# Performance work log

Hardware: AMD Instinct MI355X
Metric: run time of the kernel (lower is better)

Reference implementation:

```python
import jax, jax.numpy as jnp
import numpy as np
from math import sqrt

# ---- config (mirrors init_kwargs / input_specs) ----
B, N = 2, 2048
DIM, HEADS = 1024, 16
DH = DIM // HEADS
NUM_STEPS = 8
BETA = 1.0
SCALE = sqrt(DIM / 2 - 1)        # scale_from_dim(dim)
SCALE_HEAD = sqrt(DH / 2 - 1)    # scale_from_dim(dim_head)


def _normalize(x, eps=1e-12):
    # torch F.normalize(dim=-1): x / max(||x||, eps)
    n = jnp.linalg.norm(x, axis=-1, keepdims=True)
    return x / jnp.maximum(n, eps)


def _theta(x, J, m):
    # effective field: external field + attention-weighted coupling of magnetizations
    return x + jnp.einsum('bhij,bhjd->bhid', J, m)


def _magnetizations(theta, beta=BETA, scale=SCALE):
    # naive-MF single-site average for a vector spin on a sphere of radius `scale`
    # (steepest-descent closed form): m = beta*theta / (2 t),
    # t = (1 + sqrt(1 + beta^2 |theta|^2 / scale^2)) / 2
    # -> linear response beta*theta/2 for small fields, saturates at |m| = scale.
    h2 = jnp.sum(jnp.square(beta * theta), axis=-1, keepdims=True)
    t = 0.5 * (1.0 + jnp.sqrt(1.0 + h2 / (scale * scale)))
    return beta * theta / (2.0 * t)


def setup_inputs() -> dict:
    key = jax.random.key(0)
    k0, k1, k2, k3 = jax.random.split(key, 4)
    x = jax.random.normal(k0, (B, N, DIM), jnp.float32)
    w_qk = jax.random.normal(k1, (2 * DIM, DIM), jnp.float32) / sqrt(DIM)
    w1 = jax.random.normal(k2, (4 * DIM, DIM), jnp.float32) / sqrt(DIM)
    w2 = jax.random.normal(k3, (DIM, 4 * DIM), jnp.float32) / sqrt(4 * DIM)
    return {"x": x, "w_qk": w_qk, "w1": w1, "w2": w2}


def reference(x, w_qk, w1, w2):
    # pre_mix = Identity
    x = SCALE * _normalize(x)                         # [b,n,dim]
    qk = x @ w_qk.T                                   # [b,n,2*dim]
    q, k = jnp.split(qk, 2, axis=-1)
    ff = jax.nn.gelu(x @ w1.T, approximate=False) @ w2.T

    split = lambda t: t.reshape(B, N, HEADS, DH).transpose(0, 2, 1, 3)  # b h n d
    xh, q, k, ffh = map(split, (x, q, k, ff))
    q, k = _normalize(q), _normalize(k)
    sim = SCALE_HEAD * jnp.einsum('bhid,bhjd->bhij', q, k)
    attn = jax.nn.softmax(sim, axis=-1)               # [b,h,n,n] coupling matrix

    xf = xh + ffh                                     # external field
    # prev_mf_state.theta starts as ones(x.shape) on first call
    m0 = _magnetizations(jnp.ones_like(xf))

    # fixed-step mean-field iteration: m <- magnetizations(theta(x, attn, m))
    def body(m, _):
        m_next = _magnetizations(_theta(xf, attn, m))
        return m_next, None
    m, _ = jax.lax.scan(body, m0, None, length=NUM_STEPS)

    m = m.transpose(0, 2, 1, 3).reshape(B, N, DIM)    # merge heads
    # post_mix = Identity
    return m
```

## Files before the change

### kernel.cpp

```cpp
#include <hip/hip_runtime.h>
#include <hip/hip_bf16.h>
#include <math.h>

#define BQ 2
#define SEQ 2048
#define NDIM 1024
#define HEADS 16
#define DH 64
#define NSTEPS 8
#define SCALE 22.60530911f
#define SCALE_HEAD 5.567764363f
#define INV_SCALE2 (1.0f/511.0f)
#define EXS 8.0325527f

typedef unsigned short u16;
typedef unsigned char u8;
typedef long long i64;
typedef __attribute__((ext_vector_type(8))) short bf16x8;
typedef __attribute__((ext_vector_type(4))) float floatx4;
typedef __attribute__((ext_vector_type(2))) long long i64x2;

__device__ __forceinline__ float bf2f(u16 u) {
  union { unsigned int i; float f; } v; v.i = ((unsigned int)u) << 16; return v.f;
}
__device__ __forceinline__ u16 f2bf(float f) {
  union { float f; unsigned int i; } v; v.f = f;
  unsigned int x = v.i;
  return (u16)((x + 0x7fffu + ((x >> 16) & 1u)) >> 16);
}
#if __has_builtin(__builtin_amdgcn_exp2f)
__device__ __forceinline__ float exp2_raw(float x) { return __builtin_amdgcn_exp2f(x); }
#else
__device__ __forceinline__ float exp2_raw(float x) { return exp2f(x); }
#endif
#if __has_builtin(__builtin_amdgcn_rcpf)
__device__ __forceinline__ float rcp_raw(float x) { return __builtin_amdgcn_rcpf(x); }
#else
__device__ __forceinline__ float rcp_raw(float x) { return 1.0f/x; }
#endif

__device__ __forceinline__ float gelu_tanh(float v) {
  float v2 = v*v;
  float u = v * __builtin_fmaf(0.0356774081f, v2, 0.7978845608f);
  float t = exp2_raw(2.8853900817779268f * u);
  float th = (t - 1.0f) * rcp_raw(t + 1.0f);
  return 0.5f * v * (1.0f + th);
}

__device__ __forceinline__ int pk4_fp8(float a, float b, float c, float d) {
  int p = 0;
  p = __builtin_amdgcn_cvt_pk_fp8_f32(a, b, p, false);
  p = __builtin_amdgcn_cvt_pk_fp8_f32(c, d, p, true);
  return p;
}

#define GLD16(gp, lp) __builtin_amdgcn_global_load_lds( \
    (__attribute__((address_space(1))) void*)(gp),      \
    (__attribute__((address_space(3))) void*)(lp), 16, 0, 0)


__global__ void k_flag0(int* flag) { if (threadIdx.x == 0 && blockIdx.x == 0) *flag = 0; }

__global__ __launch_bounds__(256) void k_probe(const u16* __restrict__ x, int* __restrict__ flag) {
  int i = blockIdx.x * 256 + threadIdx.x;
  float v = bf2f(x[i]);
  if (!(fabsf(v) <= 1e4f)) atomicOr(flag, 1);
}

__global__ __launch_bounds__(256) void k_convert(const void* __restrict__ in, u16* __restrict__ outb,
                                                 const int* __restrict__ flag, int n) {
  int i = blockIdx.x * 256 + threadIdx.x;
  if (i >= n) return;
  if (*flag) outb[i] = f2bf(((const float*)in)[i]);
  else       outb[i] = ((const u16*)in)[i];
}

__global__ __launch_bounds__(256) void k_norm_scale(const u16* __restrict__ x, u16* __restrict__ xs) {
  __shared__ float red[256];
  int row = blockIdx.x;
  const u16* xr = x + (size_t)row * NDIM;
  u16* orow = xs + (size_t)row * NDIM;
  int t = threadIdx.x;
  float vals[4]; float s = 0.f;
#pragma unroll
  for (int e = 0; e < 4; e++) { float v = bf2f(xr[t + 256*e]); vals[e] = v; s += v*v; }
  red[t] = s; __syncthreads();
  for (int o = 128; o > 0; o >>= 1) { if (t < o) red[t] += red[t+o]; __syncthreads(); }
  float sc = SCALE / fmaxf(sqrtf(red[0]), 1e-12f);
#pragma unroll
  for (int e = 0; e < 4; e++) orow[t + 256*e] = f2bf(vals[e] * sc);
}

template<int OUT_BF16, int GELU, int ADDSRC>
__global__ __launch_bounds__(256) void k_gemm(const u16* __restrict__ A, const u16* __restrict__ W,
                                              float* __restrict__ Cf, u16* __restrict__ Cb,
                                              const u16* __restrict__ addsrc, int M, int N, int K) {
  __shared__ __align__(16) u16 As[128*32];
  __shared__ __align__(16) u16 Bs[128*32];
  int t = threadIdx.x;
  int w = t >> 6, L = t & 63;
  int quad = L >> 4, l15 = L & 15;
  int wr = w >> 1, wc = w & 1;
  int bm = blockIdx.x * 128, bn = blockIdx.y * 128;
  int srow = L >> 2, scol = (L & 3) * 8;
  floatx4 acc[4][4];
#pragma unroll
  for (int i = 0; i < 4; i++)
#pragma unroll
    for (int j = 0; j < 4; j++) acc[i][j] = (floatx4){0.f,0.f,0.f,0.f};

  for (int k0 = 0; k0 < K; k0 += 32) {
#pragma unroll
    for (int c = 0; c < 2; c++) {
      int r = c*64 + w*16 + srow;
      GLD16(A + (size_t)(bm + r)*K + k0 + scol, &As[(c*64 + w*16)*32]);
      GLD16(W + (size_t)(bn + r)*K + k0 + scol, &Bs[(c*64 + w*16)*32]);
    }
    __syncthreads();
    bf16x8 af[4], bfr[4];
#pragma unroll
    for (int mt = 0; mt < 4; mt++) af[mt]  = *(const bf16x8*)&As[(wr*64 + mt*16 + l15)*32 + quad*8];
#pragma unroll
    for (int nt = 0; nt < 4; nt++) bfr[nt] = *(const bf16x8*)&Bs[(wc*64 + nt*16 + l15)*32 + quad*8];
#pragma unroll
    for (int mt = 0; mt < 4; mt++)
#pragma unroll
      for (int nt = 0; nt < 4; nt++)
        acc[mt][nt] = __builtin_amdgcn_mfma_f32_16x16x32_bf16(af[mt], bfr[nt], acc[mt][nt], 0, 0, 0);
    __syncthreads();
  }
#pragma unroll
  for (int mt = 0; mt < 4; mt++)
#pragma unroll
    for (int reg = 0; reg < 4; reg++) {
      int m = bm + wr*64 + mt*16 + quad*4 + reg;
      size_t rowoff = (size_t)m * N;
#pragma unroll
      for (int nt = 0; nt < 4; nt++) {
        int n = bn + wc*64 + nt*16 + l15;
        float v = acc[mt][nt][reg];
        if (GELU) v = gelu_tanh(v);
        if (ADDSRC) v += bf2f(addsrc[rowoff + n]);
        if (OUT_BF16) Cb[rowoff + n] = f2bf(v);
        else Cf[rowoff + n] = v;
      }
    }
}

__global__ __launch_bounds__(512) void k_gemm_w2(const u16* __restrict__ A, const u16* __restrict__ W,
                                                 float* __restrict__ Cf,
                                                 const u16* __restrict__ addsrc, int M, int N, int K) {
  __shared__ __align__(16) u16 As[2][128*32];
  __shared__ __align__(16) u16 Bs[2][128*32];
  int t = threadIdx.x;
  int g = t >> 8;
  int tg = t & 255;
  int w = tg >> 6;
  int L = t & 63;
  int quad = L >> 4, l15 = L & 15;
  int wr = w >> 1, wc = w & 1;
  int bm = blockIdx.x * 128, bn = blockIdx.y * 128;
  int srow = L >> 2, scol = (L & 3) * 8;
  int kg0 = g * (K >> 1);
  floatx4 acc[4][4];
#pragma unroll
  for (int i = 0; i < 4; i++)
#pragma unroll
    for (int j = 0; j < 4; j++) acc[i][j] = (floatx4){0.f,0.f,0.f,0.f};

  for (int k0 = 0; k0 < (K >> 1); k0 += 32) {
    int kk = kg0 + k0;
#pragma unroll
    for (int c = 0; c < 2; c++) {
      int r = c*64 + w*16 + srow;
      GLD16(A + (size_t)(bm + r)*K + kk + scol, &As[g][(c*64 + w*16)*32]);
      GLD16(W + (size_t)(bn + r)*K + kk + scol, &Bs[g][(c*64 + w*16)*32]);
    }
    __syncthreads();
    bf16x8 af[4], bfr[4];
#pragma unroll
    for (int mt = 0; mt < 4; mt++) af[mt]  = *(const bf16x8*)&As[g][(wr*64 + mt*16 + l15)*32 + quad*8];
#pragma unroll
    for (int nt = 0; nt < 4; nt++) bfr[nt] = *(const bf16x8*)&Bs[g][(wc*64 + nt*16 + l15)*32 + quad*8];
#pragma unroll
    for (int mt = 0; mt < 4; mt++)
#pragma unroll
      for (int nt = 0; nt < 4; nt++)
        acc[mt][nt] = __builtin_amdgcn_mfma_f32_16x16x32_bf16(af[mt], bfr[nt], acc[mt][nt], 0, 0, 0);
    __syncthreads();
  }
  float* LFA = (float*)&As[0][0];
  float* LFB = (float*)&Bs[0][0];
#pragma unroll
  for (int r = 0; r < 2; r++) {
    float* myW = g ? LFA : LFB;
    int mtW = g ? r : (2 + r);
#pragma unroll
    for (int reg = 0; reg < 4; reg++)
#pragma unroll
      for (int nt = 0; nt < 4; nt++)
        myW[(wr*16 + quad*4 + reg)*128 + wc*64 + nt*16 + l15] = acc[mtW][nt][reg];
    __syncthreads();
    float* myR = g ? LFB : LFA;
    int mtS = g ? (2 + r) : r;
#pragma unroll
    for (int reg = 0; reg < 4; reg++) {
      int m = bm + wr*64 + mtS*16 + quad*4 + reg;
      size_t rowoff = (size_t)m * N;
#pragma unroll
      for (int nt = 0; nt < 4; nt++) {
        int n = bn + wc*64 + nt*16 + l15;
        float v = acc[mtS][nt][reg] + myR[(wr*16 + quad*4 + reg)*128 + wc*64 + nt*16 + l15];
        v += bf2f(addsrc[rowoff + n]);
        Cf[rowoff + n] = v;
      }
    }
    __syncthreads();
  }
}

__global__ __launch_bounds__(512) void k_gemm_w2ks(const u16* __restrict__ A, const u16* __restrict__ W,
                                                   float* __restrict__ pbuf, int M, int N, int K) {
  __shared__ __align__(16) u16 As[2][128*32];
  __shared__ __align__(16) u16 Bs[2][128*32];
  int t = threadIdx.x;
  int g = t >> 8;
  int tg = t & 255;
  int w = tg >> 6;
  int L = t & 63;
  int quad = L >> 4, l15 = L & 15;
  int wr = w >> 1, wc = w & 1;
  int bm = blockIdx.x * 128, bn = blockIdx.y * 128;
  int z = blockIdx.z;
  int srow = L >> 2, scol = (L & 3) * 8;
  int kg0 = z * (K >> 1) + g * (K >> 2);
  floatx4 acc[4][4];
#pragma unroll
  for (int i = 0; i < 4; i++)
#pragma unroll
    for (int j = 0; j < 4; j++) acc[i][j] = (floatx4){0.f,0.f,0.f,0.f};

  for (int k0 = 0; k0 < (K >> 2); k0 += 32) {
    int kk = kg0 + k0;
#pragma unroll
    for (int c = 0; c < 2; c++) {
      int r = c*64 + w*16 + srow;
      GLD16(A + (size_t)(bm + r)*K + kk + scol, &As[g][(c*64 + w*16)*32]);
      GLD16(W + (size_t)(bn + r)*K + kk + scol, &Bs[g][(c*64 + w*16)*32]);
    }
    __syncthreads();
    bf16x8 af[4], bfr[4];
#pragma unroll
    for (int mt = 0; mt < 4; mt++) af[mt]  = *(const bf16x8*)&As[g][(wr*64 + mt*16 + l15)*32 + quad*8];
#pragma unroll
    for (int nt = 0; nt < 4; nt++) bfr[nt] = *(const bf16x8*)&Bs[g][(wc*64 + nt*16 + l15)*32 + quad*8];
#pragma unroll
    for (int mt = 0; mt < 4; mt++)
#pragma unroll
      for (int nt = 0; nt < 4; nt++)
        acc[mt][nt] = __builtin_amdgcn_mfma_f32_16x16x32_bf16(af[mt], bfr[nt], acc[mt][nt], 0, 0, 0);
    __syncthreads();
  }
  float* LFA = (float*)&As[0][0];
  float* LFB = (float*)&Bs[0][0];
  float* pb = pbuf + (size_t)z * M * N;
#pragma unroll
  for (int r = 0; r < 2; r++) {
    float* myW = g ? LFA : LFB;
    int mtW = g ? r : (2 + r);
#pragma unroll
    for (int reg = 0; reg < 4; reg++)
#pragma unroll
      for (int nt = 0; nt < 4; nt++)
        myW[(wr*16 + quad*4 + reg)*128 + wc*64 + nt*16 + l15] = acc[mtW][nt][reg];
    __syncthreads();
    float* myR = g ? LFB : LFA;
    int mtS = g ? (2 + r) : r;
#pragma unroll
    for (int reg = 0; reg < 4; reg++) {
      int m = bm + wr*64 + mtS*16 + quad*4 + reg;
      size_t rowoff = (size_t)m * N;
#pragma unroll
      for (int nt = 0; nt < 4; nt++) {
        int n = bn + wc*64 + nt*16 + l15;
        pb[rowoff + n] = acc[mtS][nt][reg] + myR[(wr*16 + quad*4 + reg)*128 + wc*64 + nt*16 + l15];
      }
    }
    __syncthreads();
  }
}

__global__ __launch_bounds__(256) void k_w2red(const float* __restrict__ p0, const float* __restrict__ p1,
                                               const u16* __restrict__ xs, float* __restrict__ xf, int n) {
  int i = (blockIdx.x * 256 + threadIdx.x) * 4;
  if (i >= n) return;
  float4 a = *(const float4*)(p0 + i);
  float4 b = *(const float4*)(p1 + i);
  ushort4 s = *(const ushort4*)(xs + i);
  float4 o;
  o.x = a.x + b.x + bf2f(s.x);
  o.y = a.y + b.y + bf2f(s.y);
  o.z = a.z + b.z + bf2f(s.z);
  o.w = a.w + b.w + bf2f(s.w);
  *(float4*)(xf + i) = o;
}

__global__ __launch_bounds__(64) void k_headnorm(const u16* __restrict__ qkraw,
                                                 u16* __restrict__ qn, u16* __restrict__ kn) {
  int blk = blockIdx.x;
  int h = blk & (HEADS-1); int bi = blk >> 4;
  int b = bi >> 11, i = bi & (SEQ-1);
  int d = threadIdx.x;
  const u16* base = qkraw + (size_t)bi * (2*NDIM);
  float qv = bf2f(base[h*DH + d]);
  float kv = bf2f(base[NDIM + h*DH + d]);
  float qs = qv*qv, ks = kv*kv;
#pragma unroll
  for (int o = 32; o > 0; o >>= 1) { qs += __shfl_xor(qs, o); ks += __shfl_xor(ks, o); }
  size_t oidx = ((size_t)(b*HEADS + h) * SEQ + i) * DH + d;
  qn[oidx] = f2bf(qv / fmaxf(sqrtf(qs), 1e-12f));
  kn[oidx] = f2bf(kv / fmaxf(sqrtf(ks), 1e-12f));
}

__global__ __launch_bounds__(256, 4) void k_attn(const u16* __restrict__ qb, const u16* __restrict__ kb,
                                                 u8* __restrict__ attn, float* __restrict__ rowsum,
                                                 int bh0) {
  __shared__ __align__(16) u8 buf[4][4][64][16];
  __shared__ float reds[4][4][16];
  int t = threadIdx.x;
  int w = t >> 6, L = t & 63;
  int quad = L >> 4, l15 = L & 15;
  int bh_local = blockIdx.x >> 5;
  int bh = bh0 + bh_local;
  int i0blk = (blockIdx.x & 31) * 64;
  bf16x8 q0[4], q1[4];
#pragma unroll
  for (int s = 0; s < 4; s++) {
    const u16* qrow = qb + ((size_t)bh*SEQ + i0blk + s*16 + l15)*DH + quad*8;
    q0[s] = *(const bf16x8*)qrow;
    q1[s] = *(const bf16x8*)(qrow + 32);
  }
  const u16* kbase = kb + (size_t)bh*SEQ*DH;
  u8* abase = attn + ((size_t)bh_local << 22) + (size_t)(i0blk >> 4)*32768;
  float sa[4] = {0.f, 0.f, 0.f, 0.f};
  for (int g = 0; g < 8; g++) {
#pragma unroll 2
    for (int tt4 = 0; tt4 < 4; tt4++) {
      int j = w*512 + (g*4 + tt4)*16 + l15;
      const u16* krow = kbase + (size_t)j*DH + quad*8;
      bf16x8 a0 = *(const bf16x8*)krow;
      bf16x8 a1 = *(const bf16x8*)(krow + 32);
      int dl = ((tt4*2 + (quad>>1)) & 3)*16 + l15;
      int boff = (tt4>>1)*8 + (quad&1)*4;
#pragma unroll
      for (int s = 0; s < 4; s++) {
        floatx4 c = (floatx4){0.f,0.f,0.f,0.f};
        c = __builtin_amdgcn_mfma_f32_16x16x32_bf16(a0, q0[s], c, 0, 0, 0);
        c = __builtin_amdgcn_mfma_f32_16x16x32_bf16(a1, q1[s], c, 0, 0, 0);
        float e0 = exp2_raw(EXS * c[0]);
        float e1 = exp2_raw(EXS * c[1]);
        float e2 = exp2_raw(EXS * c[2]);
        float e3 = exp2_raw(EXS * c[3]);
        sa[s] += (e0 + e1) + (e2 + e3);
        *(int*)&buf[w][s][dl][boff] = pk4_fp8(e0, e1, e2, e3);
      }
    }
#pragma unroll
    for (int s = 0; s < 4; s++) {
      uint4 v = *(const uint4*)&buf[w][s][L][0];
      *(uint4*)(abase + (size_t)s*32768 + (size_t)(w*8 + g)*1024 + (size_t)L*16) = v;
    }
  }
#pragma unroll
  for (int s = 0; s < 4; s++) {
    float v = sa[s];
    v += __shfl_xor(v, 16); v += __shfl_xor(v, 32);
    if (quad == 0) reds[w][s][l15] = v;
  }
  __syncthreads();
  if (t < 64)
    rowsum[(size_t)bh_local*SEQ + i0blk + t] =
        (reds[0][t >> 4][t & 15] + reds[1][t >> 4][t & 15]) +
        (reds[2][t >> 4][t & 15] + reds[3][t >> 4][t & 15]);
}

__global__ void k_zero(float* __restrict__ o, int n) {
  int i = blockIdx.x*256 + threadIdx.x; if (i < n) o[i] = 0.f;
}

__global__ __launch_bounds__(256) void k_step0(const float* __restrict__ xf, u8* __restrict__ mT,
                                               float m0v) {
  __shared__ __align__(16) u8 tile_t[64][72];
  int bh = blockIdx.x >> 5;
  int kt2 = blockIdx.x & 31;
  int i0 = kt2 * 64;
  int b = bh >> 4, h = bh & (HEADS-1);
  int t = threadIdx.x;
  int row = t >> 2, part = t & 3;
  const float* xr = xf + ((size_t)b*SEQ + i0 + row)*NDIM + h*DH + part*16;
  float v[16]; float s = 0.f;
#pragma unroll
  for (int e = 0; e < 16; e++) { float u = xr[e] + m0v; v[e] = u; s += u*u; }
  s += __shfl_xor(s, 1); s += __shfl_xor(s, 2);
  float t2 = 0.5f*(1.0f + sqrtf(1.0f + s * INV_SCALE2));
  float inv = 1.0f/(2.0f*t2);
#pragma unroll
  for (int e = 0; e < 16; e += 4) {
    int p = pk4_fp8(v[e]*inv, v[e+1]*inv, v[e+2]*inv, v[e+3]*inv);
    tile_t[part*16 + e + 0][row] = (u8)(p & 255);
    tile_t[part*16 + e + 1][row] = (u8)((p >> 8) & 255);
    tile_t[part*16 + e + 2][row] = (u8)((p >> 16) & 255);
    tile_t[part*16 + e + 3][row] = (u8)((p >> 24) & 255);
  }
  __syncthreads();
  int nt = t >> 6, Lw = t & 63;
  i64 lo = *(const i64*)&tile_t[nt*16 + (Lw & 15)][(Lw >> 4)*8];
  i64 hi = *(const i64*)&tile_t[nt*16 + (Lw & 15)][32 + (Lw >> 4)*8];
  u8* dst = mT + ((size_t)bh << 17) + ((size_t)(nt*32 + kt2)*64 + Lw)*16;
  *(i64*)dst = lo;
  *(i64*)(dst + 8) = hi;
}

template<int LAST>
__global__ __launch_bounds__(512, 4) void k_step(const u8* __restrict__ attn, const u8* __restrict__ mT_in,
                                                 const float* __restrict__ xf,
                                                 const float* __restrict__ rowsum,
                                                 u8* __restrict__ mT_out,
                                                 float* __restrict__ out, int bh0) {
  __shared__ __align__(16) u8 ms[65536];
  int t = threadIdx.x;
  int w = t >> 6, L = t & 63;
  int quad = L >> 4, l15 = L & 15;
  int bh_local = blockIdx.x >> 4;
  int bh = bh0 + bh_local;
  int I = (blockIdx.x & 15)*8 + w;
  int b = bh >> 4, hh = bh & (HEADS-1);
  const u8* ab = attn + ((size_t)bh_local << 22) + (size_t)I*32768 + (size_t)L*16;
  const u8* mbase = mT_in + ((size_t)bh << 17) + (size_t)L*16;
  floatx4 acc[4];
#pragma unroll
  for (int j = 0; j < 4; j++) acc[j] = (floatx4){0.f,0.f,0.f,0.f};

  for (int h = 0; h < 2; h++) {
#pragma unroll
    for (int r = 0; r < 8; r++) {
      int c = r*8 + w;
      int nt = c >> 4, dk = c & 15;
      GLD16(mbase + (size_t)(nt*32 + h*16 + dk)*1024, &ms[c*1024]);
    }
    __syncthreads();
#pragma unroll 4
    for (int dk = 0; dk < 16; dk++) {
      int kt2 = h*16 + dk;
      i64x2 a  = *(const i64x2*)(ab + (size_t)kt2*1024);
      i64x2 b0 = *(const i64x2*)&ms[(size_t)(dk)*1024 + L*16];
      i64x2 b1 = *(const i64x2*)&ms[(size_t)(16 + dk)*1024 + L*16];
      i64x2 b2 = *(const i64x2*)&ms[(size_t)(32 + dk)*1024 + L*16];
      i64x2 b3 = *(const i64x2*)&ms[(size_t)(48 + dk)*1024 + L*16];
      acc[0] = __builtin_amdgcn_mfma_f32_16x16x32_fp8_fp8(a.x, b0.x, acc[0], 0, 0, 0);
      acc[1] = __builtin_amdgcn_mfma_f32_16x16x32_fp8_fp8(a.x, b1.x, acc[1], 0, 0, 0);
      acc[2] = __builtin_amdgcn_mfma_f32_16x16x32_fp8_fp8(a.x, b2.x, acc[2], 0, 0, 0);
      acc[3] = __builtin_amdgcn_mfma_f32_16x16x32_fp8_fp8(a.x, b3.x, acc[3], 0, 0, 0);
      acc[0] = __builtin_amdgcn_mfma_f32_16x16x32_fp8_fp8(a.y, b0.y, acc[0], 0, 0, 0);
      acc[1] = __builtin_amdgcn_mfma_f32_16x16x32_fp8_fp8(a.y, b1.y, acc[1], 0, 0, 0);
      acc[2] = __builtin_amdgcn_mfma_f32_16x16x32_fp8_fp8(a.y, b2.y, acc[2], 0, 0, 0);
      acc[3] = __builtin_amdgcn_mfma_f32_16x16x32_fp8_fp8(a.y, b3.y, acc[3], 0, 0, 0);
    }
    __syncthreads();
  }
  int ibase = I*16 + quad*4;
  float th[4][4]; float invr[4];
#pragma unroll
  for (int reg = 0; reg < 4; reg++) {
    float sinv = 1.0f / rowsum[(size_t)bh_local*SEQ + ibase + reg];
    size_t xoff = ((size_t)b*SEQ + ibase + reg)*NDIM + hh*DH + l15;
    float s = 0.f;
#pragma unroll
    for (int nt = 0; nt < 4; nt++) {
      float v = acc[nt][reg]*sinv + xf[xoff + nt*16];
      th[nt][reg] = v; s += v*v;
    }
    s += __shfl_xor(s, 1); s += __shfl_xor(s, 2); s += __shfl_xor(s, 4); s += __shfl_xor(s, 8);
    float tt2 = 0.5f*(1.0f + sqrtf(1.0f + s * INV_SCALE2));
    invr[reg] = 1.0f/(2.0f*tt2);
  }
  if (LAST) {
#pragma unroll
    for (int reg = 0; reg < 4; reg++) {
      size_t ooff = ((size_t)b*SEQ + ibase + reg)*NDIM + hh*DH + l15;
#pragma unroll
      for (int nt = 0; nt < 4; nt++) out[ooff + nt*16] = th[nt][reg]*invr[reg];
    }
  } else {
    int kt2o = I >> 2;
    int hf = (I >> 1) & 1;
    int lhi = ((I & 1)*2 + (quad >> 1)) & 3;
    u8* ob = mT_out + ((size_t)bh << 17) + (size_t)(lhi*16 + l15)*16 + hf*8 + (quad & 1)*4;
#pragma unroll
    for (int nt = 0; nt < 4; nt++) {
      int p = pk4_fp8(th[nt][0]*invr[0], th[nt][1]*invr[1],
                      th[nt][2]*invr[2], th[nt][3]*invr[3]);
      *(int*)(ob + (size_t)(nt*32 + kt2o)*1024) = p;
    }
  }
}

extern "C" void kernel_launch(void* const* d_in, const int* in_sizes, int n_in,
                              void* d_out, int out_size, void* d_ws, size_t ws_size,
                              hipStream_t stream) {
  const void* x    = d_in[0];
  const void* w_qk = d_in[1];
  const void* w1   = d_in[2];
  const void* w2   = d_in[3];
  float* out = (float*)d_out;

  const size_t E = (size_t)BQ*SEQ*NDIM;
  const int NW_QK = 2*NDIM*NDIM;
  const int NW1   = 4*NDIM*NDIM;
  const int NW2   = 4*NDIM*NDIM;

  char* ws = (char*)d_ws;
  size_t off = 0;
  auto alloc = [&](size_t bytes) { void* p = ws + off; off += (bytes + 255) & ~255ull; return p; };
  int*  flag = (int*)alloc(256);
  u16*  xs  = (u16*)alloc(E*2);
  u16*  qb  = (u16*)alloc(E*2);
  u16*  kb  = (u16*)alloc(E*2);
  float* xf = (float*)alloc(E*4);
  u8*   mT  = (u8*)alloc(E*2);
  float* rsum = (float*)alloc((size_t)BQ*HEADS*SEQ*4);
  u8*   mTa = mT;
  u8*   mTb = mT + E;

  char* S = ws + off;
  size_t availS = (ws_size > off) ? ws_size - off : 0;
  u16* wqkb  = (u16*)(S);
  u16* qkraw = (u16*)(S + 4194304);
  u16* w1b   = (u16*)(S + 20971520);
  u16* w2b   = (u16*)(S + 29360128);
  u16* hbuf  = (u16*)(S + 37748736);
  u8*  attn  = (u8*)(S);
  u16* xb    = (u16*)mT;

  const int rcs[6] = {4096, 2048, 1024, 512, 256, 128};
  int RC = 0;
  for (int i = 0; i < 6; i++)
    if (37748736ull + (size_t)rcs[i]*4096*2 <= availS) { RC = rcs[i]; break; }
  const int chs[6] = {32, 16, 8, 4, 2, 1};
  int CH = 0;
  for (int i = 0; i < 6; i++)
    if ((size_t)chs[i]*SEQ*SEQ <= availS) { CH = chs[i]; break; }
  if (RC == 0 || CH == 0) {
    k_zero<<<(out_size+255)/256, 256, 0, stream>>>(out, out_size);
    return;
  }
  size_t pboff = 37748736ull + (size_t)RC*4096*2;
  int use_ksp = (pboff + (size_t)RC*NDIM*8 <= availS) ? 1 : 0;
  float* pbuf = (float*)(S + pboff);

  const int M = BQ*SEQ;

  k_flag0<<<1, 64, 0, stream>>>(flag);
  k_probe<<<256, 256, 0, stream>>>((const u16*)x, flag);
  k_convert<<<(int)(E/256), 256, 0, stream>>>(x, xb, flag, (int)E);
  k_convert<<<NW_QK/256, 256, 0, stream>>>(w_qk, wqkb, flag, NW_QK);
  k_convert<<<NW1/256, 256, 0, stream>>>(w1, w1b, flag, NW1);
  k_convert<<<NW2/256, 256, 0, stream>>>(w2, w2b, flag, NW2);

  k_norm_scale<<<M, 256, 0, stream>>>(xb, xs);
  { dim3 g(M/128, 2048/128); k_gemm<1,0,0><<<g, 256, 0, stream>>>(xs, wqkb, nullptr, qkraw, nullptr, M, 2048, 1024); }
  k_headnorm<<<M*HEADS, 64, 0, stream>>>(qkraw, qb, kb);

  for (int c = 0; c < M/RC; c++) {
    const u16* xsc = xs + (size_t)c*RC*NDIM;
    { dim3 g(RC/128, 4096/128); k_gemm<1,1,0><<<g, 256, 0, stream>>>(xsc, w1b, nullptr, hbuf, nullptr, RC, 4096, 1024); }
    if (use_ksp) {
      dim3 g(RC/128, 1024/128, 2);
      k_gemm_w2ks<<<g, 512, 0, stream>>>(hbuf, w2b, pbuf, RC, 1024, 4096);
      int n = RC*NDIM;
      k_w2red<<<n/1024, 256, 0, stream>>>(pbuf, pbuf + n, xsc, xf + (size_t)c*RC*NDIM, n);
    } else {
      dim3 g(RC/128, 1024/128);
      k_gemm_w2<<<g, 512, 0, stream>>>(hbuf, w2b, xf + (size_t)c*RC*NDIM, xsc, RC, 1024, 4096);
    }
  }

  float t0 = 0.5f*(1.0f + sqrtf(1.0f + 64.0f/511.0f));
  float m0v = 1.0f/(2.0f*t0);
  k_step0<<<BQ*HEADS*32, 256, 0, stream>>>(xf, mTa, m0v);

  for (int c0 = 0; c0 < BQ*HEADS; c0 += CH) {
    k_attn<<<CH*32, 256, 0, stream>>>(qb, kb, attn, rsum, c0);
    for (int s = 1; s < NSTEPS; s++) {
      u8* src = (s & 1) ? mTa : mTb;
      u8* dst = (s & 1) ? mTb : mTa;
      if (s == NSTEPS-1)
        k_step<1><<<CH*16, 512, 0, stream>>>(attn, src, xf, rsum, nullptr, out, c0);
      else
        k_step<0><<<CH*16, 512, 0, stream>>>(attn, src, xf, rsum, dst, nullptr, c0);
    }
  }
}
```

Baseline: 554.9 us.

## Double-buffer magnetization tiles in LDS to overlap loads with MFMA

Splits the shared-memory staging of the transposed magnetization into two 32KB buffers and four K-chunks. The next chunk is prefetched with async global-to-LDS loads while MFMAs run on the current one. This is meant to hide the global load latency that the old load-sync-compute loop exposed. LDS use per block stays at 64KB, but the kernel now issues more barriers and smaller load batches.

```diff
diff --git a/kernel.cpp b/kernel.cpp
--- a/kernel.cpp
+++ b/kernel.cpp
@@ -427,7 +427,7 @@
                                                  const float* __restrict__ rowsum,
                                                  u8* __restrict__ mT_out,
                                                  float* __restrict__ out, int bh0) {
-  __shared__ __align__(16) u8 ms[65536];
+  __shared__ __align__(16) u8 ms[2][32768];
   int t = threadIdx.x;
   int w = t >> 6, L = t & 63;
   int quad = L >> 4, l15 = L & 15;
@@ -441,22 +441,31 @@
 #pragma unroll
   for (int j = 0; j < 4; j++) acc[j] = (floatx4){0.f,0.f,0.f,0.f};
 
-  for (int h = 0; h < 2; h++) {
-#pragma unroll
-    for (int r = 0; r < 8; r++) {
-      int c = r*8 + w;
-      int nt = c >> 4, dk = c & 15;
-      GLD16(mbase + (size_t)(nt*32 + h*16 + dk)*1024, &ms[c*1024]);
-    }
-    __syncthreads();
+#pragma unroll
+  for (int r = 0; r < 4; r++) {
+    int c = w*4 + r;
+    int nt = c >> 3, dk8 = c & 7;
+    GLD16(mbase + (size_t)(nt*32 + dk8)*1024, &ms[0][c*1024]);
+  }
+  __syncthreads();
+  int cur = 0;
+  for (int g = 0; g < 4; g++) {
+    if (g < 3) {
+#pragma unroll
+      for (int r = 0; r < 4; r++) {
+        int c = w*4 + r;
+        int nt = c >> 3, dk8 = c & 7;
+        GLD16(mbase + (size_t)(nt*32 + (g+1)*8 + dk8)*1024, &ms[cur^1][c*1024]);
+      }
+    }
 #pragma unroll 4
-    for (int dk = 0; dk < 16; dk++) {
-      int kt2 = h*16 + dk;
+    for (int dk = 0; dk < 8; dk++) {
+      int kt2 = g*8 + dk;
       i64x2 a  = *(const i64x2*)(ab + (size_t)kt2*1024);
-      i64x2 b0 = *(const i64x2*)&ms[(size_t)(dk)*1024 + L*16];
-      i64x2 b1 = *(const i64x2*)&ms[(size_t)(16 + dk)*1024 + L*16];
-      i64x2 b2 = *(const i64x2*)&ms[(size_t)(32 + dk)*1024 + L*16];
-      i64x2 b3 = *(const i64x2*)&ms[(size_t)(48 + dk)*1024 + L*16];
+      i64x2 b0 = *(const i64x2*)&ms[cur][(size_t)(dk)*1024 + L*16];
+      i64x2 b1 = *(const i64x2*)&ms[cur][(size_t)(8 + dk)*1024 + L*16];
+      i64x2 b2 = *(const i64x2*)&ms[cur][(size_t)(16 + dk)*1024 + L*16];
+      i64x2 b3 = *(const i64x2*)&ms[cur][(size_t)(24 + dk)*1024 + L*16];
       acc[0] = __builtin_amdgcn_mfma_f32_16x16x32_fp8_fp8(a.x, b0.x, acc[0], 0, 0, 0);
       acc[1] = __builtin_amdgcn_mfma_f32_16x16x32_fp8_fp8(a.x, b1.x, acc[1], 0, 0, 0);
       acc[2] = __builtin_amdgcn_mfma_f32_16x16x32_fp8_fp8(a.x, b2.x, acc[2], 0, 0, 0);
@@ -467,6 +476,7 @@
       acc[3] = __builtin_amdgcn_mfma_f32_16x16x32_fp8_fp8(a.y, b3.y, acc[3], 0, 0, 0);
     }
     __syncthreads();
+    cur ^= 1;
   }
   int ibase = I*16 + quad*4;
   float th[4][4]; float invr[4];
```

New measurement: 568.0 us. +2.4%, slower.
